# Performance work log

Hardware: AMD Instinct MI355X
Metric: run time of the kernel (lower is better)

Reference implementation:

```python
import jax, jax.numpy as jnp
import numpy as np

ALPHA = 0.2  # leaky relu slope
NEG = -9e15


def setup_inputs() -> dict:
    key = jax.random.key(0)
    k1, k2, k3, k4 = jax.random.split(key, 4)
    B, N, Fin, Fout = 16, 2048, 256, 256
    h = jax.random.normal(k1, (B, N, Fin), dtype=jnp.float32)
    adj = jax.random.randint(k2, (B, N, N), 0, 2, dtype=jnp.int32)
    # xavier_uniform with gain 1.414 on [B, Fin, Fout] (fan over last two dims)
    limW = 1.414 * np.sqrt(6.0 / (Fin + Fout))
    W = jax.random.uniform(k3, (B, Fin, Fout), minval=-limW, maxval=limW, dtype=jnp.float32)
    lima = 1.414 * np.sqrt(6.0 / (2 * Fout + 1))
    a = jax.random.uniform(k4, (B, 2 * Fout, 1), minval=-lima, maxval=lima, dtype=jnp.float32)
    return {"h": h, "adj": adj, "W": W, "a": a}


def reference(h, adj, W, a):
    Fout = W.shape[-1]
    Wh = jnp.einsum('bnf,bfo->bno', h, W)                 # [B,N,Fout]
    Wh1 = jnp.einsum('bno,bo->bn', Wh, a[:, :Fout, 0])    # [B,N]
    Wh2 = jnp.einsum('bno,bo->bn', Wh, a[:, Fout:, 0])    # [B,N]
    e = Wh1[:, :, None] + Wh2[:, None, :]                 # [B,N,N]
    e = jnp.where(e > 0, e, ALPHA * e)                    # leaky relu
    att = jnp.where(adj > 0, e, NEG)
    att = jax.nn.softmax(att, axis=1)                     # NOTE: dim=1 as in source
    # dropout: eval mode -> identity
    h_prime = jnp.einsum('bij,bjo->bio', att, Wh)         # [B,N,Fout]
    return jax.nn.elu(h_prime)                            # concat=True
```

## Files before the change

kernel.cpp:

```cpp
#include <hip/hip_runtime.h>
#include <hip/hip_bf16.h>

typedef unsigned short u16;
typedef __attribute__((ext_vector_type(8))) short bf16x8;
typedef __attribute__((ext_vector_type(4))) float f32x4;

#define NB 16
#define NN 2048
#define FF 256
#define LOG2E 1.4426950408889634f

__device__ __forceinline__ u16 f2bf(float x) {
    union { float f; unsigned u; } v; v.f = x;
    unsigned r = v.u + 0x7fffu + ((v.u >> 16) & 1u);
    return (u16)(r >> 16);
}

#define GLD_LDS(g, l) __builtin_amdgcn_global_load_lds((const __attribute__((address_space(1))) void*)(g), (__attribute__((address_space(3))) void*)(l), 16, 0, 0)

__global__ __launch_bounds__(256) void k_prep_w(const float* __restrict__ W, const float* __restrict__ a,
                                                u16* __restrict__ WT, float* __restrict__ u1, float* __restrict__ u2) {
    int b = blockIdx.y, t = threadIdx.x;
    __shared__ float a1s[FF], a2s[FF];
    a1s[t] = a[b*2*FF + t];
    a2s[t] = a[b*2*FF + FF + t];
    __syncthreads();
    int f = blockIdx.x*64 + (t >> 2);
    int o0 = (t & 3) * 64;
    const float* wrow = W + (size_t)(b*FF + f)*FF + o0;
    u16* wtb = WT + (size_t)b*FF*FF;
    float s1 = 0.f, s2 = 0.f;
#pragma unroll
    for (int c = 0; c < 16; ++c) {
        float4 v = *(const float4*)(wrow + c*4);
        int o = o0 + c*4;
        s1 += v.x*a1s[o] + v.y*a1s[o+1] + v.z*a1s[o+2] + v.w*a1s[o+3];
        s2 += v.x*a2s[o] + v.y*a2s[o+1] + v.z*a2s[o+2] + v.w*a2s[o+3];
        wtb[(size_t)(o+0)*FF + f] = f2bf(v.x);
        wtb[(size_t)(o+1)*FF + f] = f2bf(v.y);
        wtb[(size_t)(o+2)*FF + f] = f2bf(v.z);
        wtb[(size_t)(o+3)*FF + f] = f2bf(v.w);
    }
    s1 += __shfl_xor(s1, 1); s1 += __shfl_xor(s1, 2);
    s2 += __shfl_xor(s2, 1); s2 += __shfl_xor(s2, 2);
    if ((t & 3) == 0) { u1[b*FF + f] = s1; u2[b*FF + f] = s2; }
}

__global__ __launch_bounds__(256) void k_prep_h(const float* __restrict__ h, const float* __restrict__ u1,
                                                const float* __restrict__ u2, u16* __restrict__ hbf,
                                                float* __restrict__ Wh1, float* __restrict__ Wh2) {
    int b = blockIdx.y, t = threadIdx.x;
    __shared__ float u1s[FF], u2s[FF];
    u1s[t] = u1[b*FF + t];
    u2s[t] = u2[b*FF + t];
    __syncthreads();
    int wave = t >> 6, lane = t & 63;
    int i = blockIdx.x*4 + wave;
    size_t rowoff = ((size_t)(b*NN + i))*FF + lane*4;
    float4 v = *(const float4*)(h + rowoff);
    u16 h0 = f2bf(v.x), h1 = f2bf(v.y), h2 = f2bf(v.z), h3 = f2bf(v.w);
    unsigned p0 = (unsigned)h0 | ((unsigned)h1 << 16);
    unsigned p1 = (unsigned)h2 | ((unsigned)h3 << 16);
    uint2 pk; pk.x = p0; pk.y = p1;
    *(uint2*)(hbf + rowoff) = pk;
    int o = lane*4;
    float s1 = v.x*u1s[o] + v.y*u1s[o+1] + v.z*u1s[o+2] + v.w*u1s[o+3];
    float s2 = v.x*u2s[o] + v.y*u2s[o+1] + v.z*u2s[o+2] + v.w*u2s[o+3];
#pragma unroll
    for (int off = 32; off > 0; off >>= 1) { s1 += __shfl_xor(s1, off); s2 += __shfl_xor(s2, off); }
    if (lane == 0) { Wh1[b*NN + i] = s1; Wh2[b*NN + i] = s2; }
}

__global__ __launch_bounds__(256) void k_gemm1(const u16* __restrict__ WT, const u16* __restrict__ hbf,
                                               u16* __restrict__ WhT) {
    int b = blockIdx.z;
    int o0 = blockIdx.y * 64;
    int i0 = blockIdx.x * 256;
    int t = threadIdx.x, lane = t & 63, w = t >> 6;
    __shared__ alignas(16) u16 At[64*64];
    __shared__ alignas(16) u16 Btl[256*64];
    const u16* WTb = WT + (size_t)b*FF*FF;
    const u16* hb  = hbf + (size_t)b*NN*FF;

    f32x4 acc[4][4];
#pragma unroll
    for (int x = 0; x < 4; ++x)
#pragma unroll
        for (int y = 0; y < 4; ++y) acc[x][y] = (f32x4)0.f;

    for (int kk = 0; kk < 4; ++kk) {
        int k0 = kk*64;
#pragma unroll
        for (int is = 0; is < 2; ++is) {
            int s = is*256 + t;
            int row = s >> 3, jbp = s & 7;
            int jbl = jbp ^ (row & 7);
            GLD_LDS(WTb + (size_t)(o0+row)*FF + k0 + jbl*8, &At[s*8]);
        }
#pragma unroll
        for (int is = 0; is < 8; ++is) {
            int s = is*256 + t;
            int row = s >> 3, jbp = s & 7;
            int jbl = jbp ^ (row & 7);
            GLD_LDS(hb + (size_t)(i0+row)*FF + k0 + jbl*8, &Btl[s*8]);
        }
        __syncthreads();
#pragma unroll
        for (int kc = 0; kc < 2; ++kc) {
            int jl = kc*4 + (lane >> 4);
            bf16x8 af[4], bfr[4];
#pragma unroll
            for (int mi = 0; mi < 4; ++mi) {
                int r = mi*16 + (lane & 15);
                af[mi] = *(const bf16x8*)&At[r*64 + (jl ^ (r & 7))*8];
            }
#pragma unroll
            for (int ni = 0; ni < 4; ++ni) {
                int r = w*64 + ni*16 + (lane & 15);
                bfr[ni] = *(const bf16x8*)&Btl[r*64 + (jl ^ (r & 7))*8];
            }
#pragma unroll
            for (int mi = 0; mi < 4; ++mi)
#pragma unroll
                for (int ni = 0; ni < 4; ++ni)
                    acc[mi][ni] = __builtin_amdgcn_mfma_f32_16x16x32_bf16(af[mi], bfr[ni], acc[mi][ni], 0, 0, 0);
        }
        __syncthreads();
    }
    u16* Wo = WhT + (size_t)b*FF*NN;
#pragma unroll
    for (int mi = 0; mi < 4; ++mi)
#pragma unroll
        for (int ni = 0; ni < 4; ++ni) {
            int i = i0 + w*64 + ni*16 + (lane & 15);
#pragma unroll
            for (int rr = 0; rr < 4; ++rr) {
                int o = o0 + mi*16 + (lane >> 4)*4 + rr;
                Wo[(size_t)o*NN + i] = f2bf(acc[mi][ni][rr]);
            }
        }
}

__global__ __launch_bounds__(256) void k_colsum(const int* __restrict__ adj, const float* __restrict__ Wh1,
                                                const float* __restrict__ Wh2, float* __restrict__ pS,
                                                unsigned long long* __restrict__ packed) {
    int b = blockIdx.z, ic = blockIdx.y, jt = blockIdx.x;
    int t = threadIdx.x, lane = t & 63, wave = t >> 6;
    __shared__ float wh1s[256];
    int ibase = ic*256;
    wh1s[t] = Wh1[b*NN + ibase + t];
    __syncthreads();
    int j = jt*256 + t;
    float wh2j = Wh2[b*NN + j];
    const int* acol = adj + (size_t)b*NN*NN + (size_t)ibase*NN + j;
    unsigned long long* prow = packed + ((size_t)(b*NN + ibase))*32 + jt*4 + wave;
    float s = 0.f;
    for (int ii = 0; ii < 256; ii += 8) {
        int v[8];
#pragma unroll
        for (int r = 0; r < 8; ++r) v[r] = acol[(size_t)(ii + r)*NN];
#pragma unroll
        for (int r = 0; r < 8; ++r) {
            bool p = v[r] > 0;
            unsigned long long m = __ballot(p);
            if (lane == 0) prow[(size_t)(ii + r)*32] = m;
            float tt = wh1s[ii + r] + wh2j;
            float lr = fmaxf(tt, 0.2f*tt);
            float e = __expf(lr);
            s += p ? e : 0.f;
        }
    }
    pS[((size_t)(b*8 + ic))*NN + j] = s;
}

__global__ __launch_bounds__(256) void k_combine(const float* __restrict__ pS, float* __restrict__ lns2) {
    int idx = blockIdx.x*256 + threadIdx.x;
    int b = idx >> 11, j = idx & 2047;
    float s = 0.f;
#pragma unroll
    for (int c = 0; c < 8; ++c) s += pS[((size_t)(b*8 + c))*NN + j];
    lns2[idx] = (s > 0.f) ? log2f(s) : __builtin_inff();
}

__global__ __launch_bounds__(512) void k_gemm3(const u16* __restrict__ WhT, const unsigned long long* __restrict__ packed,
                                               const float* __restrict__ Wh1, const float* __restrict__ Wh2,
                                               const float* __restrict__ lns2, float* __restrict__ out) {
    int b = blockIdx.y;
    int i0 = blockIdx.x * 128;
    int t = threadIdx.x, lane = t & 63, wave = t >> 6;
    int wm = wave >> 2, wn = wave & 3;
    __shared__ alignas(16) u16 At[2][128*64];
    __shared__ alignas(16) u16 Bt[2][256*64];
    __shared__ float wh2s[NN];
    __shared__ float lss[NN];
    __shared__ float wh1s[128];

#pragma unroll
    for (int c = 0; c < 4; ++c) {
        int idx = c*512 + t;
        wh2s[idx] = Wh2[b*NN + idx];
        lss[idx]  = lns2[b*NN + idx];
    }
    if (t < 128) wh1s[t] = Wh1[b*NN + i0 + t];

    const u16* Wo = WhT + (size_t)b*FF*NN;
    const u16* pk = (const u16*)(packed + ((size_t)b*NN)*32);
    int rA = t >> 2, qA = t & 3;

    __syncthreads();

    f32x4 acc[4][4];
#pragma unroll
    for (int x = 0; x < 4; ++x)
#pragma unroll
        for (int y = 0; y < 4; ++y) acc[x][y] = (f32x4)0.f;

    auto stageB = [&](int kk, int bbuf) {
        int k0 = kk*64;
#pragma unroll
        for (int is = 0; is < 4; ++is) {
            int s = is*512 + t;
            int row = s >> 3, jbp = s & 7;
            int jbl = jbp ^ (row & 7);
            GLD_LDS(Wo + (size_t)row*NN + k0 + jbl*8, &Bt[bbuf][s*8]);
        }
    };
    auto genA = [&](int kk, int bbuf) {
        unsigned mask = pk[(size_t)(i0 + rA)*128 + kk*4 + qA];
        float wh1r = wh1s[rA];
        int jb = kk*64 + qA*16;
        const float4* w2p = (const float4*)&wh2s[jb];
        const float4* lsp = (const float4*)&lss[jb];
        union { u16 u[16]; bf16x8 v[2]; } ob;
#pragma unroll
        for (int c = 0; c < 4; ++c) {
            float4 w2 = w2p[c];
            float4 ls = lsp[c];
            float xs[4] = {w2.x, w2.y, w2.z, w2.w};
            float lv[4] = {ls.x, ls.y, ls.z, ls.w};
#pragma unroll
            for (int e = 0; e < 4; ++e) {
                float tt = wh1r + xs[e];
                float lr = fmaxf(tt, 0.2f*tt);
                float pe = exp2f(lr*LOG2E - lv[e]);
                int bit = (mask >> (c*4 + e)) & 1;
                ob.u[c*4 + e] = bit ? f2bf(pe) : (u16)0;
            }
        }
        int rx = rA & 7;
#pragma unroll
        for (int c2 = 0; c2 < 2; ++c2)
            *(bf16x8*)&At[bbuf][rA*64 + ((qA*2 + c2) ^ rx)*8] = ob.v[c2];
    };

    int bb = 0;
    stageB(0, 0);
    genA(0, 0);
    __syncthreads();

    for (int kk = 0; kk < 32; ++kk) {
        int nb = bb ^ 1;
        if (kk + 1 < 32) { stageB(kk+1, nb); genA(kk+1, nb); }
#pragma unroll
        for (int kc = 0; kc < 2; ++kc) {
            int jl = kc*4 + (lane >> 4);
            bf16x8 af[4], bfr[4];
#pragma unroll
            for (int mi = 0; mi < 4; ++mi) {
                int r = wm*64 + mi*16 + (lane & 15);
                af[mi] = *(const bf16x8*)&At[bb][r*64 + (jl ^ (r & 7))*8];
            }
#pragma unroll
            for (int ni = 0; ni < 4; ++ni) {
                int r = wn*64 + ni*16 + (lane & 15);
                bfr[ni] = *(const bf16x8*)&Bt[bb][r*64 + (jl ^ (r & 7))*8];
            }
#pragma unroll
            for (int mi = 0; mi < 4; ++mi)
#pragma unroll
                for (int ni = 0; ni < 4; ++ni)
                    acc[mi][ni] = __builtin_amdgcn_mfma_f32_16x16x32_bf16(af[mi], bfr[ni], acc[mi][ni], 0, 0, 0);
        }
        __syncthreads();
        bb = nb;
    }

    float* ob2 = out + ((size_t)b*NN)*FF;
#pragma unroll
    for (int mi = 0; mi < 4; ++mi)
#pragma unroll
        for (int ni = 0; ni < 4; ++ni) {
            int o = wn*64 + ni*16 + (lane & 15);
#pragma unroll
            for (int rr = 0; rr < 4; ++rr) {
                int i = i0 + wm*64 + mi*16 + (lane >> 4)*4 + rr;
                float x = acc[mi][ni][rr];
                float y = (x > 0.f) ? x : (exp2f(x*LOG2E) - 1.f);
                ob2[(size_t)i*FF + o] = y;
            }
        }
}

extern "C" void kernel_launch(void* const* d_in, const int* in_sizes, int n_in,
                              void* d_out, int out_size, void* d_ws, size_t ws_size,
                              hipStream_t stream) {
    const float* h   = (const float*)d_in[0];
    const int*   adj = (const int*)d_in[1];
    const float* W   = (const float*)d_in[2];
    const float* a   = (const float*)d_in[3];
    float* out = (float*)d_out;

    char* w = (char*)d_ws;
    const size_t MB = 1u << 20;
    u16* WT  = (u16*)(w + 0);
    u16* hbf = (u16*)(w + 2*MB);
    u16* WhT = (u16*)(w + 18*MB);
    unsigned long long* packed = (unsigned long long*)(w + 34*MB);
    float* pS  = (float*)(w + 42*MB);
    float* Wh1 = (float*)(w + 43*MB);
    float* Wh2 = (float*)(w + 43*MB + 131072);
    float* lns = (float*)(w + 43*MB + 2*131072);
    float* u1  = (float*)(w + 43*MB + 3*131072);
    float* u2  = (float*)(w + 43*MB + 3*131072 + 16384);

    k_prep_w<<<dim3(4, 16), 256, 0, stream>>>(W, a, WT, u1, u2);
    k_prep_h<<<dim3(512, 16), 256, 0, stream>>>(h, u1, u2, hbf, Wh1, Wh2);
    k_gemm1<<<dim3(8, 4, 16), 256, 0, stream>>>(WT, hbf, WhT);
    k_colsum<<<dim3(8, 8, 16), 256, 0, stream>>>(adj, Wh1, Wh2, pS, packed);
    k_combine<<<128, 256, 0, stream>>>(pS, lns);
    k_gemm3<<<dim3(16, 16), 512, 0, stream>>>(WhT, packed, Wh1, Wh2, lns, out);
}
```

Before: 164.5 us.

## Fuse combine into attention GEMM and interleave staging with MFMA clusters

Removes the separate combine kernel by computing per-column log-sum inside the final GEMM's prologue, and pre-scales Wh1/Wh2 by log2(e) so exponentials use exp2 directly. The final GEMM's main loop is restructured into four MFMA quadrants interleaved with half-sized B staging and A generation, using barriers and s_setprio to overlap memory/ALU work with matrix ops. Blocks are remapped with a swizzled 1D grid to group batches across chiplets. The prologue now redundantly reduces partial sums per block and adds extra barriers per iteration.

New measurement: 174.7 us. 6.2% more time.

```diff
diff --git a/kernel.cpp b/kernel.cpp
--- a/kernel.cpp
+++ b/kernel.cpp
@@ -2,6 +2,7 @@
 #include <hip/hip_bf16.h>
 
 typedef unsigned short u16;
+typedef unsigned long long u64;
 typedef __attribute__((ext_vector_type(8))) short bf16x8;
 typedef __attribute__((ext_vector_type(4))) float f32x4;
 
@@ -68,7 +69,7 @@
     float s2 = v.x*u2s[o] + v.y*u2s[o+1] + v.z*u2s[o+2] + v.w*u2s[o+3];
 #pragma unroll
     for (int off = 32; off > 0; off >>= 1) { s1 += __shfl_xor(s1, off); s2 += __shfl_xor(s2, off); }
-    if (lane == 0) { Wh1[b*NN + i] = s1; Wh2[b*NN + i] = s2; }
+    if (lane == 0) { Wh1[b*NN + i] = s1*LOG2E; Wh2[b*NN + i] = s2*LOG2E; }
 }
 
 __global__ __launch_bounds__(256) void k_gemm1(const u16* __restrict__ WT, const u16* __restrict__ hbf,
@@ -143,7 +144,7 @@
 
 __global__ __launch_bounds__(256) void k_colsum(const int* __restrict__ adj, const float* __restrict__ Wh1,
                                                 const float* __restrict__ Wh2, float* __restrict__ pS,
-                                                unsigned long long* __restrict__ packed) {
+                                                u64* __restrict__ packed) {
     int b = blockIdx.z, ic = blockIdx.y, jt = blockIdx.x;
     int t = threadIdx.x, lane = t & 63, wave = t >> 6;
     __shared__ float wh1s[256];
@@ -153,7 +154,7 @@
     int j = jt*256 + t;
     float wh2j = Wh2[b*NN + j];
     const int* acol = adj + (size_t)b*NN*NN + (size_t)ibase*NN + j;
-    unsigned long long* prow = packed + ((size_t)(b*NN + ibase))*32 + jt*4 + wave;
+    u64* prow = packed + ((size_t)(b*NN + ibase))*32 + jt*4 + wave;
     float s = 0.f;
     for (int ii = 0; ii < 256; ii += 8) {
         int v[8];
@@ -162,31 +163,24 @@
 #pragma unroll
         for (int r = 0; r < 8; ++r) {
             bool p = v[r] > 0;
-            unsigned long long m = __ballot(p);
+            u64 m = __ballot(p);
             if (lane == 0) prow[(size_t)(ii + r)*32] = m;
             float tt = wh1s[ii + r] + wh2j;
             float lr = fmaxf(tt, 0.2f*tt);
-            float e = __expf(lr);
+            float e = exp2f(lr);
             s += p ? e : 0.f;
         }
     }
     pS[((size_t)(b*8 + ic))*NN + j] = s;
 }
 
-__global__ __launch_bounds__(256) void k_combine(const float* __restrict__ pS, float* __restrict__ lns2) {
-    int idx = blockIdx.x*256 + threadIdx.x;
-    int b = idx >> 11, j = idx & 2047;
-    float s = 0.f;
-#pragma unroll
-    for (int c = 0; c < 8; ++c) s += pS[((size_t)(b*8 + c))*NN + j];
-    lns2[idx] = (s > 0.f) ? log2f(s) : __builtin_inff();
-}
-
-__global__ __launch_bounds__(512) void k_gemm3(const u16* __restrict__ WhT, const unsigned long long* __restrict__ packed,
-                                               const float* __restrict__ Wh1, const float* __restrict__ Wh2,
-                                               const float* __restrict__ lns2, float* __restrict__ out) {
-    int b = blockIdx.y;
-    int i0 = blockIdx.x * 128;
+__global__ __launch_bounds__(512, 1) void k_gemm3(const u16* __restrict__ WhT, const u64* __restrict__ packed,
+                                                  const float* __restrict__ Wh1, const float* __restrict__ Wh2,
+                                                  const float* __restrict__ pS, float* __restrict__ out) {
+    int bid = blockIdx.x;
+    int nid = (bid & 7)*32 + (bid >> 3);
+    int b  = nid >> 4;
+    int i0 = (nid & 15) * 128;
     int t = threadIdx.x, lane = t & 63, wave = t >> 6;
     int wm = wave >> 2, wn = wave & 3;
     __shared__ alignas(16) u16 At[2][128*64];
@@ -199,7 +193,10 @@
     for (int c = 0; c < 4; ++c) {
         int idx = c*512 + t;
         wh2s[idx] = Wh2[b*NN + idx];
-        lss[idx]  = lns2[b*NN + idx];
+        float s = 0.f;
+#pragma unroll
+        for (int cc = 0; cc < 8; ++cc) s += pS[((size_t)(b*8 + cc))*NN + idx];
+        lss[idx] = (s > 0.f) ? log2f(s) : __builtin_inff();
     }
     if (t < 128) wh1s[t] = Wh1[b*NN + i0 + t];
 
@@ -207,83 +204,119 @@
     const u16* pk = (const u16*)(packed + ((size_t)b*NN)*32);
     int rA = t >> 2, qA = t & 3;
 
-    __syncthreads();
-
     f32x4 acc[4][4];
 #pragma unroll
     for (int x = 0; x < 4; ++x)
 #pragma unroll
         for (int y = 0; y < 4; ++y) acc[x][y] = (f32x4)0.f;
 
-    auto stageB = [&](int kk, int bbuf) {
+    auto stageB_half = [&](int kk, int bbuf, int hf) {
         int k0 = kk*64;
 #pragma unroll
-        for (int is = 0; is < 4; ++is) {
+        for (int is = hf*2; is < hf*2 + 2; ++is) {
             int s = is*512 + t;
             int row = s >> 3, jbp = s & 7;
             int jbl = jbp ^ (row & 7);
             GLD_LDS(Wo + (size_t)row*NN + k0 + jbl*8, &Bt[bbuf][s*8]);
         }
     };
-    auto genA = [&](int kk, int bbuf) {
-        unsigned mask = pk[(size_t)(i0 + rA)*128 + kk*4 + qA];
+    auto genA_half = [&](int kk, int bbuf, int hf) {
+        unsigned mask = (unsigned)(pk[(size_t)(i0 + rA)*128 + kk*4 + qA]) >> (hf*8);
         float wh1r = wh1s[rA];
-        int jb = kk*64 + qA*16;
-        const float4* w2p = (const float4*)&wh2s[jb];
-        const float4* lsp = (const float4*)&lss[jb];
-        union { u16 u[16]; bf16x8 v[2]; } ob;
-#pragma unroll
-        for (int c = 0; c < 4; ++c) {
-            float4 w2 = w2p[c];
-            float4 ls = lsp[c];
-            float xs[4] = {w2.x, w2.y, w2.z, w2.w};
-            float lv[4] = {ls.x, ls.y, ls.z, ls.w};
-#pragma unroll
-            for (int e = 0; e < 4; ++e) {
-                float tt = wh1r + xs[e];
-                float lr = fmaxf(tt, 0.2f*tt);
-                float pe = exp2f(lr*LOG2E - lv[e]);
-                int bit = (mask >> (c*4 + e)) & 1;
-                ob.u[c*4 + e] = bit ? f2bf(pe) : (u16)0;
-            }
-        }
-        int rx = rA & 7;
-#pragma unroll
-        for (int c2 = 0; c2 < 2; ++c2)
-            *(bf16x8*)&At[bbuf][rA*64 + ((qA*2 + c2) ^ rx)*8] = ob.v[c2];
+        int jb = kk*64 + qA*16 + hf*8;
+        float4 w2a = *(const float4*)&wh2s[jb];
+        float4 w2b = *(const float4*)&wh2s[jb+4];
+        float4 la  = *(const float4*)&lss[jb];
+        float4 lb  = *(const float4*)&lss[jb+4];
+        float xs[8] = {w2a.x, w2a.y, w2a.z, w2a.w, w2b.x, w2b.y, w2b.z, w2b.w};
+        float lv[8] = {la.x, la.y, la.z, la.w, lb.x, lb.y, lb.z, lb.w};
+        union { u16 u[8]; bf16x8 v; } ob;
+#pragma unroll
+        for (int e = 0; e < 8; ++e) {
+            float tt = wh1r + xs[e];
+            float lr = fmaxf(tt, 0.2f*tt);
+            float pe = exp2f(lr - lv[e]);
+            ob.u[e] = ((mask >> e) & 1) ? f2bf(pe) : (u16)0;
+        }
+        *(bf16x8*)&At[bbuf][rA*64 + (((qA*2 + hf) ^ (rA & 7))*8)] = ob.v;
     };
+    auto rdA = [&](int bbuf, int mi, int kc) -> bf16x8 {
+        int r = wm*64 + mi*16 + (lane & 15);
+        int jl = kc*4 + (lane >> 4);
+        return *(const bf16x8*)&At[bbuf][r*64 + ((jl ^ (r & 7))*8)];
+    };
+    auto rdB = [&](int bbuf, int ni, int kc) -> bf16x8 {
+        int r = wn*64 + ni*16 + (lane & 15);
+        int jl = kc*4 + (lane >> 4);
+        return *(const bf16x8*)&Bt[bbuf][r*64 + ((jl ^ (r & 7))*8)];
+    };
+
+#define MM(mi, ni, af, bf) acc[mi][ni] = __builtin_amdgcn_mfma_f32_16x16x32_bf16(af, bf, acc[mi][ni], 0, 0, 0)
+
+    __syncthreads();
+    stageB_half(0, 0, 0); stageB_half(0, 0, 1);
+    genA_half(0, 0, 0);  genA_half(0, 0, 1);
+    __syncthreads();
 
     int bb = 0;
-    stageB(0, 0);
-    genA(0, 0);
-    __syncthreads();
-
     for (int kk = 0; kk < 32; ++kk) {
         int nb = bb ^ 1;
-        if (kk + 1 < 32) { stageB(kk+1, nb); genA(kk+1, nb); }
-#pragma unroll
-        for (int kc = 0; kc < 2; ++kc) {
-            int jl = kc*4 + (lane >> 4);
-            bf16x8 af[4], bfr[4];
-#pragma unroll
-            for (int mi = 0; mi < 4; ++mi) {
-                int r = wm*64 + mi*16 + (lane & 15);
-                af[mi] = *(const bf16x8*)&At[bb][r*64 + (jl ^ (r & 7))*8];
-            }
-#pragma unroll
-            for (int ni = 0; ni < 4; ++ni) {
-                int r = wn*64 + ni*16 + (lane & 15);
-                bfr[ni] = *(const bf16x8*)&Bt[bb][r*64 + (jl ^ (r & 7))*8];
-            }
-#pragma unroll
-            for (int mi = 0; mi < 4; ++mi)
-#pragma unroll
-                for (int ni = 0; ni < 4; ++ni)
-                    acc[mi][ni] = __builtin_amdgcn_mfma_f32_16x16x32_bf16(af[mi], bfr[ni], acc[mi][ni], 0, 0, 0);
-        }
+        bool pf = (kk + 1 < 32);
+        bf16x8 aR0[2][2], aR1[2][2], bR0[2][2], bR1[2][2];
+
+#pragma unroll
+        for (int x = 0; x < 2; ++x)
+#pragma unroll
+            for (int kc = 0; kc < 2; ++kc) { aR0[x][kc] = rdA(bb, x, kc); bR0[x][kc] = rdB(bb, x, kc); }
+        if (pf) stageB_half(kk+1, nb, 0);
+        __builtin_amdgcn_s_barrier();
+        __builtin_amdgcn_s_setprio(1);
+        MM(0,0,aR0[0][0],bR0[0][0]); MM(0,1,aR0[0][0],bR0[1][0]);
+        MM(1,0,aR0[1][0],bR0[0][0]); MM(1,1,aR0[1][0],bR0[1][0]);
+        MM(0,0,aR0[0][1],bR0[0][1]); MM(0,1,aR0[0][1],bR0[1][1]);
+        MM(1,0,aR0[1][1],bR0[0][1]); MM(1,1,aR0[1][1],bR0[1][1]);
+        __builtin_amdgcn_s_setprio(0);
+        __builtin_amdgcn_s_barrier();
+
+#pragma unroll
+        for (int x = 0; x < 2; ++x)
+#pragma unroll
+            for (int kc = 0; kc < 2; ++kc) bR1[x][kc] = rdB(bb, 2 + x, kc);
+        if (pf) stageB_half(kk+1, nb, 1);
+        __builtin_amdgcn_s_barrier();
+        __builtin_amdgcn_s_setprio(1);
+        MM(0,2,aR0[0][0],bR1[0][0]); MM(0,3,aR0[0][0],bR1[1][0]);
+        MM(1,2,aR0[1][0],bR1[0][0]); MM(1,3,aR0[1][0],bR1[1][0]);
+        MM(0,2,aR0[0][1],bR1[0][1]); MM(0,3,aR0[0][1],bR1[1][1]);
+        MM(1,2,aR0[1][1],bR1[0][1]); MM(1,3,aR0[1][1],bR1[1][1]);
+        __builtin_amdgcn_s_setprio(0);
+        __builtin_amdgcn_s_barrier();
+
+#pragma unroll
+        for (int x = 0; x < 2; ++x)
+#pragma unroll
+            for (int kc = 0; kc < 2; ++kc) aR1[x][kc] = rdA(bb, 2 + x, kc);
+        if (pf) genA_half(kk+1, nb, 0);
+        __builtin_amdgcn_s_barrier();
+        __builtin_amdgcn_s_setprio(1);
+        MM(2,0,aR1[0][0],bR0[0][0]); MM(2,1,aR1[0][0],bR0[1][0]);
+        MM(3,0,aR1[1][0],bR0[0][0]); MM(3,1,aR1[1][0],bR0[1][0]);
+        MM(2,0,aR1[0][1],bR0[0][1]); MM(2,1,aR1[0][1],bR0[1][1]);
+        MM(3,0,aR1[1][1],bR0[0][1]); MM(3,1,aR1[1][1],bR0[1][1]);
+        __builtin_amdgcn_s_setprio(0);
+        __builtin_amdgcn_s_barrier();
+
+        if (pf) genA_half(kk+1, nb, 1);
+        __builtin_amdgcn_s_setprio(1);
+        MM(2,2,aR1[0][0],bR1[0][0]); MM(2,3,aR1[0][0],bR1[1][0]);
+        MM(3,2,aR1[1][0],bR1[0][0]); MM(3,3,aR1[1][0],bR1[1][0]);
+        MM(2,2,aR1[0][1],bR1[0][1]); MM(2,3,aR1[0][1],bR1[1][1]);
+        MM(3,2,aR1[1][1],bR1[0][1]); MM(3,3,aR1[1][1],bR1[1][1]);
+        __builtin_amdgcn_s_setprio(0);
         __syncthreads();
         bb = nb;
     }
+#undef MM
 
     float* ob2 = out + ((size_t)b*NN)*FF;
 #pragma unroll
@@ -315,11 +348,10 @@
     u16* WT  = (u16*)(w + 0);
     u16* hbf = (u16*)(w + 2*MB);
     u16* WhT = (u16*)(w + 18*MB);
-    unsigned long long* packed = (unsigned long long*)(w + 34*MB);
+    u64* packed = (u64*)(w + 34*MB);
     float* pS  = (float*)(w + 42*MB);
     float* Wh1 = (float*)(w + 43*MB);
     float* Wh2 = (float*)(w + 43*MB + 131072);
-    float* lns = (float*)(w + 43*MB + 2*131072);
     float* u1  = (float*)(w + 43*MB + 3*131072);
     float* u2  = (float*)(w + 43*MB + 3*131072 + 16384);
 
@@ -327,6 +359,5 @@
     k_prep_h<<<dim3(512, 16), 256, 0, stream>>>(h, u1, u2, hbf, Wh1, Wh2);
     k_gemm1<<<dim3(8, 4, 16), 256, 0, stream>>>(WT, hbf, WhT);
     k_colsum<<<dim3(8, 8, 16), 256, 0, stream>>>(adj, Wh1, Wh2, pS, packed);
-    k_combine<<<128, 256, 0, stream>>>(pS, lns);
-    k_gemm3<<<dim3(16, 16), 512, 0, stream>>>(WhT, packed, Wh1, Wh2, lns, out);
-}
+    k_gemm3<<<dim3(256, 1), 512, 0, stream>>>(WhT, packed, Wh1, Wh2, pS, out);
+}
```
